# Kernel optimization log

Hardware: AMD Instinct MI355X
Metric: run time of the kernel (lower is better)

Reference implementation:

```python
import jax, jax.numpy as jnp
import numpy as np

DIM = 768
N_HEADS = 12
HEAD_DIM = DIM // N_HEADS
SCALE = HEAD_DIM ** -0.5


def setup_inputs() -> dict:
    key = jax.random.key(0)
    ks = jax.random.split(key, 5)
    x = jax.random.normal(ks[0], (8, 1024, DIM), dtype=jnp.float32)
    w_qkv = jax.random.normal(ks[1], (DIM, 3 * DIM), dtype=jnp.float32) * (DIM ** -0.5)
    b_qkv = jnp.zeros((3 * DIM,), dtype=jnp.float32)
    w_proj = jax.random.normal(ks[2], (DIM, DIM), dtype=jnp.float32) * (DIM ** -0.5)
    b_proj = jnp.zeros((DIM,), dtype=jnp.float32)
    return {"x": x, "w_qkv": w_qkv, "b_qkv": b_qkv, "w_proj": w_proj, "b_proj": b_proj}


def reference(x, w_qkv, b_qkv, w_proj, b_proj):
    B, N, _ = x.shape
    qkv = x @ w_qkv + b_qkv                       # [B, N, 3*DIM]
    qkv = qkv.reshape(B, N, 3, N_HEADS, HEAD_DIM)
    q = qkv[:, :, 0].transpose(0, 2, 1, 3)        # [B, H, N, D]
    k = qkv[:, :, 1].transpose(0, 2, 1, 3)
    v = qkv[:, :, 2].transpose(0, 2, 1, 3)
    attn = jnp.einsum('bhnd,bhmd->bhnm', q, k) * SCALE
    attn = jax.nn.softmax(attn, axis=-1)
    out = jnp.einsum('bhnm,bhmd->bhnd', attn, v)  # [B, H, N, D]
    out = out.transpose(0, 2, 1, 3).reshape(B, N, DIM)
    return out @ w_proj + b_proj
```

## Files before the change

kernel.cpp:

```cpp
#include <hip/hip_runtime.h>
#include <hip/hip_bf16.h>

#define NHEADS 12
#define HDIM   64
#define SEQ    1024
#define NBATCH 8
#define MODELD 768
#define QKVD   2304
#define BHEADS (NBATCH * NHEADS)

typedef __attribute__((ext_vector_type(8))) short          bf16x8;
typedef __attribute__((ext_vector_type(8))) unsigned short u16x8;
typedef __attribute__((ext_vector_type(4))) unsigned short u16x4;
typedef __attribute__((ext_vector_type(4))) float          f32x4;

static __device__ __forceinline__ unsigned short f2bf(float f) {
  unsigned int u = __float_as_uint(f);
  u += 0x7fffu + ((u >> 16) & 1u);
  return (unsigned short)(u >> 16);
}

static __device__ __forceinline__ unsigned int pk2(float x, float y) {
  __hip_bfloat162 h = __float22bfloat162_rn(make_float2(x, y));
  return *(unsigned int*)&h;
}

static __device__ __forceinline__ void gld_lds16(const void* g, void* l) {
  __builtin_amdgcn_global_load_lds((const __attribute__((address_space(1))) void*)g,
                                   (__attribute__((address_space(3))) void*)l, 16, 0, 0);
}

#define QSC 0.18033688f

__global__ __launch_bounds__(256) void convert_x(
    const float* __restrict__ in, unsigned short* __restrict__ out) {
  const int i = (blockIdx.x * 256 + threadIdx.x) * 8;
  const float4 a0 = *(const float4*)(in + i);
  const float4 a1 = *(const float4*)(in + i + 4);
  union { unsigned int u[4]; u16x8 v; } w;
  w.u[0] = pk2(a0.x, a0.y); w.u[1] = pk2(a0.z, a0.w);
  w.u[2] = pk2(a1.x, a1.y); w.u[3] = pk2(a1.z, a1.w);
  *(u16x8*)(out + i) = w.v;
}

__global__ __launch_bounds__(256) void transpose_f32_to_bf16(
    const float* __restrict__ in, unsigned short* __restrict__ out, int R, int C) {
  __shared__ float t[32][33];
  const int c0 = blockIdx.x * 32, r0 = blockIdx.y * 32;
  const int lr = threadIdx.x >> 3;
  const int lc = (threadIdx.x & 7) * 4;
  const float* p = in + (size_t)(r0 + lr) * C + c0 + lc;
  float4 v = *(const float4*)p;
  t[lr][lc]     = v.x;
  t[lr][lc + 1] = v.y;
  t[lr][lc + 2] = v.z;
  t[lr][lc + 3] = v.w;
  __syncthreads();
  unsigned short* q = out + (size_t)(c0 + lr) * R + r0 + lc;
  q[0] = f2bf(t[lc][lr]);
  q[1] = f2bf(t[lc + 1][lr]);
  q[2] = f2bf(t[lc + 2][lr]);
  q[3] = f2bf(t[lc + 3][lr]);
}

__global__ __launch_bounds__(512) void gemm_qkv(
    const unsigned short* __restrict__ Xb, const unsigned short* __restrict__ WT,
    const float* __restrict__ bias,
    unsigned short* __restrict__ Qo, unsigned short* __restrict__ Ko,
    unsigned short* __restrict__ VTo) {
  __shared__ __align__(16) unsigned short smem[49152];
  const int tid  = threadIdx.x;
  const int lane = tid & 63;
  const int wave = tid >> 6;
  int flat = blockIdx.x;
  flat = (flat & 7) * 72 + (flat >> 3);
  const int m0 = (flat / 18) * 256;
  const int n0 = (flat % 18) * 128;
  const int wrm = (wave >> 1) * 64;
  const int wcn = (wave & 1) * 64;
  const int srow = lane >> 3;
  const int scol = (((lane & 7) ^ srow) << 4);
  const int fr = lane & 15;
  const int fq = lane >> 4;
  const int swz = (fr & 7) << 4;

  const char* Ab = (const char*)(Xb + (size_t)m0 * MODELD);
  const char* Bb = (const char*)(WT + (size_t)n0 * MODELD);

  f32x4 acc[4][4] = {};

  auto stage = [&](int buf, int k0) {
#pragma unroll
    for (int u = 0; u < 4; ++u) {
      const int i = wave * 4 + u;
      const size_t roff = (size_t)(i * 8 + srow) * (MODELD * 2) + k0 * 2 + scol;
      gld_lds16(Ab + roff, (char*)smem + buf * 32768 + i * 1024);
    }
#pragma unroll
    for (int u = 0; u < 2; ++u) {
      const int i = wave * 2 + u;
      const size_t roff = (size_t)(i * 8 + srow) * (MODELD * 2) + k0 * 2 + scol;
      gld_lds16(Bb + roff, (char*)smem + 65536 + buf * 16384 + i * 1024);
    }
  };

  stage(0, 0);

  for (int t = 0; t < 12; ++t) {
    const int cur = t & 1;
    if (t < 11) {
      stage(cur ^ 1, (t + 1) * 64);
      asm volatile("s_waitcnt vmcnt(6)" ::: "memory");
    } else {
      asm volatile("s_waitcnt vmcnt(0)" ::: "memory");
    }
    __builtin_amdgcn_s_barrier();

    const char* Ac = (const char*)smem + cur * 32768;
    const char* Bc = (const char*)smem + 65536 + cur * 16384;
#pragma unroll
    for (int c = 0; c < 2; ++c) {
      const int cb = (c * 64 + fq * 16);
      bf16x8 af[4], bfr[4];
#pragma unroll
      for (int i = 0; i < 4; ++i) {
        af[i]  = *(const bf16x8*)(Ac + (wrm + i * 16 + fr) * 128 + (cb ^ swz));
        bfr[i] = *(const bf16x8*)(Bc + (wcn + i * 16 + fr) * 128 + (cb ^ swz));
      }
      __builtin_amdgcn_s_setprio(1);
#pragma unroll
      for (int i = 0; i < 4; ++i)
#pragma unroll
        for (int j = 0; j < 4; ++j)
          acc[i][j] = __builtin_amdgcn_mfma_f32_16x16x32_bf16(af[i], bfr[j], acc[i][j], 0, 0, 0);
      __builtin_amdgcn_s_setprio(0);
    }
    __builtin_amdgcn_s_barrier();
  }

  const int s = n0 / MODELD;
  if (s < 2) {
    const float qs = (s == 0) ? QSC : 1.0f;
#pragma unroll
    for (int i = 0; i < 4; ++i) {
#pragma unroll
      for (int j = 0; j < 4; ++j) {
        const int col = n0 + wcn + j * 16 + fr;
        const int rem = col - s * MODELD;
        const int h = rem >> 6, d = rem & 63;
        const float bv = bias[col];
#pragma unroll
        for (int r = 0; r < 4; ++r) {
          const int row = m0 + wrm + i * 16 + fq * 4 + r;
          const int b = row >> 10, n = row & 1023;
          const int bh = b * NHEADS + h;
          const unsigned short val = f2bf((acc[i][j][r] + bv) * qs);
          if (s == 0) Qo[((size_t)bh * SEQ + n) * HDIM + d] = val;
          else        Ko[((size_t)bh * SEQ + n) * HDIM + d] = val;
        }
      }
    }
  } else {
    unsigned short* T = smem + wave * 4608;
#pragma unroll
    for (int i = 0; i < 4; ++i) {
#pragma unroll
      for (int j = 0; j < 4; ++j) {
        const int col = n0 + wcn + j * 16 + fr;
        const float bv = bias[col];
        const int dl = j * 16 + fr;
        union { unsigned int u[2]; u16x4 v; } pk;
        pk.u[0] = pk2(acc[i][j][0] + bv, acc[i][j][1] + bv);
        pk.u[1] = pk2(acc[i][j][2] + bv, acc[i][j][3] + bv);
        *(u16x4*)&T[dl * 72 + i * 16 + fq * 4] = pk.v;
      }
    }
    asm volatile("s_waitcnt lgkmcnt(0)" ::: "memory");
    const int h  = (n0 + wcn - 2 * MODELD) >> 6;
    const int rowb = m0 + wrm;
    const int b  = rowb >> 10, nq = rowb & 1023;
    const int bh = b * NHEADS + h;
    unsigned short* Vb = VTo + ((size_t)bh * HDIM) * SEQ + nq;
#pragma unroll
    for (int u = 0; u < 8; ++u) {
      const int d  = u * 8 + (lane >> 3);
      const int qc = (lane & 7) * 8;
      u16x8 v = *(const u16x8*)&T[d * 72 + qc];
      *(u16x8*)(Vb + (size_t)d * SEQ + qc) = v;
    }
  }
}

__global__ __launch_bounds__(256, 3) void attn_fused(
    const unsigned short* __restrict__ Q, const unsigned short* __restrict__ K,
    const unsigned short* __restrict__ VT, unsigned short* __restrict__ AO) {
  __shared__ unsigned short Ks[2][64][64];
  __shared__ unsigned short Vs[2][64][64];

  const int tid  = threadIdx.x;
  const int lane = tid & 63;
  const int wave = tid >> 6;

  const int flat = blockIdx.y * 8 + blockIdx.x;
  const int xcd = flat & 7, j = flat >> 3;
  const int bh = xcd * 12 + (j >> 3);
  const int qb = j & 7;
  const int b = bh / NHEADS, h = bh % NHEADS;
  const int q0 = qb * 128 + wave * 32;

  const unsigned short* Qp = Q  + (size_t)bh * SEQ * HDIM;
  const unsigned short* Kp = K  + (size_t)bh * SEQ * HDIM;
  const unsigned short* Vp = VT + (size_t)bh * HDIM * SEQ;

  const int fr = lane & 15;
  const int fq = lane >> 4;
  const int swz = (fr & 7) << 4;

  bf16x8 qf[2][2];
#pragma unroll
  for (int g = 0; g < 2; ++g)
#pragma unroll
    for (int c = 0; c < 2; ++c)
      qf[g][c] = *(const bf16x8*)(Qp + (size_t)(q0 + g * 16 + fr) * HDIM + c * 32 + fq * 8);

  const int srow_lo = (lane >> 3);
  const int scx = (((lane & 7) ^ srow_lo) << 4);

  f32x4 acc[2][4] = {};
  f32x4 accl[2] = {};
  bf16x8 ones;
#pragma unroll
  for (int i = 0; i < 8; ++i) ones[i] = (short)0x3F80;

  auto stage = [&](int buf, int kv0) {
    const char* Kb = (const char*)Kp + (size_t)kv0 * 128;
    const char* Vb = (const char*)Vp + (size_t)kv0 * 2;
    char* dK = (char*)&Ks[buf][0][0];
    char* dV = (char*)&Vs[buf][0][0];
#pragma unroll
    for (int u = 0; u < 2; ++u) {
      const int i = wave * 2 + u;
      const int r0 = i * 8 + srow_lo;
      gld_lds16(Kb + (size_t)r0 * 128  + scx, dK + i * 1024);
      gld_lds16(Vb + (size_t)r0 * 2048 + scx, dV + i * 1024);
    }
  };

  stage(0, 0);

  for (int t = 0; t < SEQ / 64; ++t) {
    const int cur = t & 1;
    if (t < SEQ / 64 - 1) {
      stage(cur ^ 1, (t + 1) * 64);
      asm volatile("s_waitcnt vmcnt(4)" ::: "memory");
    } else {
      asm volatile("s_waitcnt vmcnt(0)" ::: "memory");
    }
    __builtin_amdgcn_s_barrier();

    const char* Kt = (const char*)&Ks[cur][0][0];
    const char* Vt = (const char*)&Vs[cur][0][0];

    bf16x8 kf[4][2];
#pragma unroll
    for (int ng = 0; ng < 4; ++ng)
#pragma unroll
      for (int c = 0; c < 2; ++c)
        kf[ng][c] = *(const bf16x8*)(Kt + (ng * 16 + fr) * 128 + ((c * 64 + fq * 16) ^ swz));

    f32x4 S[2][4] = {};
    __builtin_amdgcn_s_setprio(1);
#pragma unroll
    for (int g = 0; g < 2; ++g)
#pragma unroll
      for (int ng = 0; ng < 4; ++ng)
#pragma unroll
        for (int c = 0; c < 2; ++c)
          S[g][ng] = __builtin_amdgcn_mfma_f32_16x16x32_bf16(kf[ng][c], qf[g][c], S[g][ng], 0, 0, 0);
    __builtin_amdgcn_s_setprio(0);

    bf16x8 pf[2][2];
#pragma unroll
    for (int g = 0; g < 2; ++g) {
      unsigned int u[4][2];
#pragma unroll
      for (int ng = 0; ng < 4; ++ng) {
        const float p0 = __builtin_amdgcn_exp2f(S[g][ng][0]);
        const float p1 = __builtin_amdgcn_exp2f(S[g][ng][1]);
        const float p2 = __builtin_amdgcn_exp2f(S[g][ng][2]);
        const float p3 = __builtin_amdgcn_exp2f(S[g][ng][3]);
        u[ng][0] = pk2(p0, p1);
        u[ng][1] = pk2(p2, p3);
      }
#pragma unroll
      for (int c = 0; c < 2; ++c) {
        union { unsigned int w[4]; bf16x8 v; } pp;
#pragma unroll
        for (int d2 = 0; d2 < 2; ++d2) {
          unsigned int e = u[2 * c][d2], o = u[2 * c + 1][d2];
          asm("v_permlane32_swap_b32 %0, %1" : "+v"(e), "+v"(o));
          asm("v_permlane16_swap_b32 %0, %1" : "+v"(e), "+v"(o));
          pp.w[d2] = e;
          pp.w[2 + d2] = o;
        }
        pf[g][c] = pp.v;
      }
    }

    bf16x8 vf[4][2];
#pragma unroll
    for (int df = 0; df < 4; ++df)
#pragma unroll
      for (int c = 0; c < 2; ++c)
        vf[df][c] = *(const bf16x8*)(Vt + (df * 16 + fr) * 128 + ((c * 64 + fq * 16) ^ swz));

    __builtin_amdgcn_s_setprio(1);
#pragma unroll
    for (int g = 0; g < 2; ++g) {
#pragma unroll
      for (int df = 0; df < 4; ++df)
#pragma unroll
        for (int c = 0; c < 2; ++c)
          acc[g][df] = __builtin_amdgcn_mfma_f32_16x16x32_bf16(pf[g][c], vf[df][c], acc[g][df], 0, 0, 0);
#pragma unroll
      for (int c = 0; c < 2; ++c)
        accl[g] = __builtin_amdgcn_mfma_f32_16x16x32_bf16(pf[g][c], ones, accl[g], 0, 0, 0);
    }
    __builtin_amdgcn_s_setprio(0);

    __builtin_amdgcn_s_barrier();
  }

#pragma unroll
  for (int g = 0; g < 2; ++g) {
#pragma unroll
    for (int r = 0; r < 4; ++r) {
      const float inv = 1.0f / accl[g][r];
      const int q = q0 + g * 16 + fq * 4 + r;
      unsigned short* outp = AO + ((size_t)b * SEQ + q) * MODELD + h * HDIM;
#pragma unroll
      for (int df = 0; df < 4; ++df)
        outp[df * 16 + fr] = f2bf(acc[g][df][r] * inv);
    }
  }
}

__global__ __launch_bounds__(512) void gemm_proj(
    const unsigned short* __restrict__ A, const unsigned short* __restrict__ WT,
    const float* __restrict__ bias, float* __restrict__ Out) {
  __shared__ __align__(16) unsigned short smem[49152];
  const int tid  = threadIdx.x;
  const int lane = tid & 63;
  const int wave = tid >> 6;
  int flat = blockIdx.x;
  flat = (flat & 7) * 24 + (flat >> 3);
  const int m0 = (flat / 6) * 256;
  const int n0 = (flat % 6) * 128;
  const int wrm = (wave >> 1) * 64;
  const int wcn = (wave & 1) * 64;
  const int srow = lane >> 3;
  const int scol = (((lane & 7) ^ srow) << 4);
  const int fr = lane & 15;
  const int fq = lane >> 4;
  const int swz = (fr & 7) << 4;

  const char* Ab = (const char*)(A  + (size_t)m0 * MODELD);
  const char* Bb = (const char*)(WT + (size_t)n0 * MODELD);

  f32x4 acc[4][4] = {};

  auto stage = [&](int buf, int k0) {
#pragma unroll
    for (int u = 0; u < 4; ++u) {
      const int i = wave * 4 + u;
      const size_t roff = (size_t)(i * 8 + srow) * (MODELD * 2) + k0 * 2 + scol;
      gld_lds16(Ab + roff, (char*)smem + buf * 32768 + i * 1024);
    }
#pragma unroll
    for (int u = 0; u < 2; ++u) {
      const int i = wave * 2 + u;
      const size_t roff = (size_t)(i * 8 + srow) * (MODELD * 2) + k0 * 2 + scol;
      gld_lds16(Bb + roff, (char*)smem + 65536 + buf * 16384 + i * 1024);
    }
  };

  stage(0, 0);

  for (int t = 0; t < 12; ++t) {
    const int cur = t & 1;
    if (t < 11) {
      stage(cur ^ 1, (t + 1) * 64);
      asm volatile("s_waitcnt vmcnt(6)" ::: "memory");
    } else {
      asm volatile("s_waitcnt vmcnt(0)" ::: "memory");
    }
    __builtin_amdgcn_s_barrier();

    const char* Ac = (const char*)smem + cur * 32768;
    const char* Bc = (const char*)smem + 65536 + cur * 16384;
#pragma unroll
    for (int c = 0; c < 2; ++c) {
      const int cb = (c * 64 + fq * 16);
      bf16x8 af[4], bfr[4];
#pragma unroll
      for (int i = 0; i < 4; ++i) {
        af[i]  = *(const bf16x8*)(Ac + (wrm + i * 16 + fr) * 128 + (cb ^ swz));
        bfr[i] = *(const bf16x8*)(Bc + (wcn + i * 16 + fr) * 128 + (cb ^ swz));
      }
      __builtin_amdgcn_s_setprio(1);
#pragma unroll
      for (int i = 0; i < 4; ++i)
#pragma unroll
        for (int j = 0; j < 4; ++j)
          acc[i][j] = __builtin_amdgcn_mfma_f32_16x16x32_bf16(af[i], bfr[j], acc[i][j], 0, 0, 0);
      __builtin_amdgcn_s_setprio(0);
    }
    __builtin_amdgcn_s_barrier();
  }

#pragma unroll
  for (int i = 0; i < 4; ++i) {
#pragma unroll
    for (int j = 0; j < 4; ++j) {
      const int col = n0 + wcn + j * 16 + fr;
      const float bv = bias[col];
#pragma unroll
      for (int r = 0; r < 4; ++r) {
        const int row = m0 + wrm + i * 16 + fq * 4 + r;
        Out[(size_t)row * MODELD + col] = acc[i][j][r] + bv;
      }
    }
  }
}

extern "C" void kernel_launch(void* const* d_in, const int* in_sizes, int n_in,
                              void* d_out, int out_size, void* d_ws, size_t ws_size,
                              hipStream_t stream) {
  const float* x      = (const float*)d_in[0];
  const float* w_qkv  = (const float*)d_in[1];
  const float* b_qkv  = (const float*)d_in[2];
  const float* w_proj = (const float*)d_in[3];
  const float* b_proj = (const float*)d_in[4];
  float* out = (float*)d_out;

  unsigned short* ws = (unsigned short*)d_ws;
  unsigned short* wqkvT  = ws;
  unsigned short* wprojT = wqkvT + (size_t)QKVD * MODELD;
  unsigned short* Qw     = wprojT + (size_t)MODELD * MODELD;
  unsigned short* Kw     = Qw + (size_t)BHEADS * SEQ * HDIM;
  unsigned short* VTw    = Kw + (size_t)BHEADS * SEQ * HDIM;
  unsigned short* AO     = VTw + (size_t)BHEADS * SEQ * HDIM;
  unsigned short* Xb     = AO + (size_t)NBATCH * SEQ * MODELD;

  convert_x<<<dim3((NBATCH * SEQ * MODELD) / (256 * 8)), 256, 0, stream>>>(x, Xb);
  transpose_f32_to_bf16<<<dim3(QKVD / 32, MODELD / 32), 256, 0, stream>>>(
      w_qkv, wqkvT, MODELD, QKVD);
  transpose_f32_to_bf16<<<dim3(MODELD / 32, MODELD / 32), 256, 0, stream>>>(
      w_proj, wprojT, MODELD, MODELD);
  gemm_qkv<<<dim3((QKVD / 128) * ((NBATCH * SEQ) / 256)), 512, 0, stream>>>(
      Xb, wqkvT, b_qkv, Qw, Kw, VTw);
  attn_fused<<<dim3(SEQ / 128, BHEADS), 256, 0, stream>>>(Qw, Kw, VTw, AO);
  gemm_proj<<<dim3((MODELD / 128) * ((NBATCH * SEQ) / 256)), 512, 0, stream>>>(
      AO, wprojT, b_proj, out);
}
```

Before: 110.4 us.

## Triple-buffer LDS pipelines in GEMMs and attention; merge prep kernels into one launch

The QKV GEMM, the projection GEMM and the attention kernel move from double-buffered to triple-buffered LDS staging. Each iteration now prefetches two tiles ahead and drops one of its two barriers, since the buffer being refilled was read one iteration earlier. The three preprocessing kernels (convert x to bf16, transpose the two weight matrices) are folded into a single launch that dispatches on block index, saving two kernel launches. The cost is more LDS per block: the GEMMs go to about 144KB, which still fits one 512-thread block per CU, and attention goes to 48KB per block.

```diff
diff --git a/kernel.cpp b/kernel.cpp
--- a/kernel.cpp
+++ b/kernel.cpp
@@ -32,23 +32,13 @@
 
 #define QSC 0.18033688f
 
-__global__ __launch_bounds__(256) void convert_x(
-    const float* __restrict__ in, unsigned short* __restrict__ out) {
-  const int i = (blockIdx.x * 256 + threadIdx.x) * 8;
-  const float4 a0 = *(const float4*)(in + i);
-  const float4 a1 = *(const float4*)(in + i + 4);
-  union { unsigned int u[4]; u16x8 v; } w;
-  w.u[0] = pk2(a0.x, a0.y); w.u[1] = pk2(a0.z, a0.w);
-  w.u[2] = pk2(a1.x, a1.y); w.u[3] = pk2(a1.z, a1.w);
-  *(u16x8*)(out + i) = w.v;
-}
-
-__global__ __launch_bounds__(256) void transpose_f32_to_bf16(
-    const float* __restrict__ in, unsigned short* __restrict__ out, int R, int C) {
+static __device__ __forceinline__ void transpose_body(
+    const float* __restrict__ in, unsigned short* __restrict__ out,
+    int R, int C, int bx, int by, int tid) {
   __shared__ float t[32][33];
-  const int c0 = blockIdx.x * 32, r0 = blockIdx.y * 32;
-  const int lr = threadIdx.x >> 3;
-  const int lc = (threadIdx.x & 7) * 4;
+  const int c0 = bx * 32, r0 = by * 32;
+  const int lr = tid >> 3;
+  const int lc = (tid & 7) * 4;
   const float* p = in + (size_t)(r0 + lr) * C + c0 + lc;
   float4 v = *(const float4*)p;
   t[lr][lc]     = v.x;
@@ -63,12 +53,35 @@
   q[3] = f2bf(t[lc + 3][lr]);
 }
 
+__global__ __launch_bounds__(256) void prep(
+    const float* __restrict__ x, unsigned short* __restrict__ Xb,
+    const float* __restrict__ w_qkv, unsigned short* __restrict__ wqkvT,
+    const float* __restrict__ w_proj, unsigned short* __restrict__ wprojT) {
+  const int id = blockIdx.x;
+  const int tid = threadIdx.x;
+  if (id < 3072) {
+    const int i = (id * 256 + tid) * 8;
+    const float4 a0 = *(const float4*)(x + i);
+    const float4 a1 = *(const float4*)(x + i + 4);
+    union { unsigned int u[4]; u16x8 v; } w;
+    w.u[0] = pk2(a0.x, a0.y); w.u[1] = pk2(a0.z, a0.w);
+    w.u[2] = pk2(a1.x, a1.y); w.u[3] = pk2(a1.z, a1.w);
+    *(u16x8*)(Xb + i) = w.v;
+  } else if (id < 4800) {
+    const int u = id - 3072;
+    transpose_body(w_qkv, wqkvT, MODELD, QKVD, u % 72, u / 72, tid);
+  } else {
+    const int u = id - 4800;
+    transpose_body(w_proj, wprojT, MODELD, MODELD, u % 24, u / 24, tid);
+  }
+}
+
 __global__ __launch_bounds__(512) void gemm_qkv(
     const unsigned short* __restrict__ Xb, const unsigned short* __restrict__ WT,
     const float* __restrict__ bias,
     unsigned short* __restrict__ Qo, unsigned short* __restrict__ Ko,
     unsigned short* __restrict__ VTo) {
-  __shared__ __align__(16) unsigned short smem[49152];
+  __shared__ __align__(16) unsigned short smem[73728];
   const int tid  = threadIdx.x;
   const int lane = tid & 63;
   const int wave = tid >> 6;
@@ -100,24 +113,25 @@
     for (int u = 0; u < 2; ++u) {
       const int i = wave * 2 + u;
       const size_t roff = (size_t)(i * 8 + srow) * (MODELD * 2) + k0 * 2 + scol;
-      gld_lds16(Bb + roff, (char*)smem + 65536 + buf * 16384 + i * 1024);
+      gld_lds16(Bb + roff, (char*)smem + 98304 + buf * 16384 + i * 1024);
     }
   };
 
   stage(0, 0);
-
+  stage(1, 64);
+
+  int cur = 0;
   for (int t = 0; t < 12; ++t) {
-    const int cur = t & 1;
-    if (t < 11) {
-      stage(cur ^ 1, (t + 1) * 64);
-      asm volatile("s_waitcnt vmcnt(6)" ::: "memory");
-    } else {
-      asm volatile("s_waitcnt vmcnt(0)" ::: "memory");
-    }
+    if (t < 11) asm volatile("s_waitcnt vmcnt(6)" ::: "memory");
+    else        asm volatile("s_waitcnt vmcnt(0)" ::: "memory");
     __builtin_amdgcn_s_barrier();
+    if (t < 10) {
+      int sb = cur + 2; if (sb >= 3) sb -= 3;
+      stage(sb, (t + 2) * 64);
+    }
 
     const char* Ac = (const char*)smem + cur * 32768;
-    const char* Bc = (const char*)smem + 65536 + cur * 16384;
+    const char* Bc = (const char*)smem + 98304 + cur * 16384;
 #pragma unroll
     for (int c = 0; c < 2; ++c) {
       const int cb = (c * 64 + fq * 16);
@@ -135,8 +149,9 @@
           acc[i][j] = __builtin_amdgcn_mfma_f32_16x16x32_bf16(af[i], bfr[j], acc[i][j], 0, 0, 0);
       __builtin_amdgcn_s_setprio(0);
     }
-    __builtin_amdgcn_s_barrier();
-  }
+    cur = (cur == 2) ? 0 : cur + 1;
+  }
+  __builtin_amdgcn_s_barrier();
 
   const int s = n0 / MODELD;
   if (s < 2) {
@@ -194,8 +209,7 @@
 __global__ __launch_bounds__(256, 3) void attn_fused(
     const unsigned short* __restrict__ Q, const unsigned short* __restrict__ K,
     const unsigned short* __restrict__ VT, unsigned short* __restrict__ AO) {
-  __shared__ unsigned short Ks[2][64][64];
-  __shared__ unsigned short Vs[2][64][64];
+  __shared__ __align__(16) unsigned short smem[24576];
 
   const int tid  = threadIdx.x;
   const int lane = tid & 63;
@@ -235,31 +249,30 @@
   auto stage = [&](int buf, int kv0) {
     const char* Kb = (const char*)Kp + (size_t)kv0 * 128;
     const char* Vb = (const char*)Vp + (size_t)kv0 * 2;
-    char* dK = (char*)&Ks[buf][0][0];
-    char* dV = (char*)&Vs[buf][0][0];
 #pragma unroll
     for (int u = 0; u < 2; ++u) {
       const int i = wave * 2 + u;
       const int r0 = i * 8 + srow_lo;
-      gld_lds16(Kb + (size_t)r0 * 128  + scx, dK + i * 1024);
-      gld_lds16(Vb + (size_t)r0 * 2048 + scx, dV + i * 1024);
+      gld_lds16(Kb + (size_t)r0 * 128  + scx, (char*)smem + buf * 8192 + i * 1024);
+      gld_lds16(Vb + (size_t)r0 * 2048 + scx, (char*)smem + 24576 + buf * 8192 + i * 1024);
     }
   };
 
   stage(0, 0);
-
+  stage(1, 64);
+
+  int cur = 0;
   for (int t = 0; t < SEQ / 64; ++t) {
-    const int cur = t & 1;
-    if (t < SEQ / 64 - 1) {
-      stage(cur ^ 1, (t + 1) * 64);
-      asm volatile("s_waitcnt vmcnt(4)" ::: "memory");
-    } else {
-      asm volatile("s_waitcnt vmcnt(0)" ::: "memory");
-    }
+    if (t < SEQ / 64 - 1) asm volatile("s_waitcnt vmcnt(4)" ::: "memory");
+    else                  asm volatile("s_waitcnt vmcnt(0)" ::: "memory");
     __builtin_amdgcn_s_barrier();
-
-    const char* Kt = (const char*)&Ks[cur][0][0];
-    const char* Vt = (const char*)&Vs[cur][0][0];
+    if (t < SEQ / 64 - 2) {
+      int sb = cur + 2; if (sb >= 3) sb -= 3;
+      stage(sb, (t + 2) * 64);
+    }
+
+    const char* Kt = (const char*)smem + cur * 8192;
+    const char* Vt = (const char*)smem + 24576 + cur * 8192;
 
     bf16x8 kf[4][2];
 #pragma unroll
@@ -328,7 +341,7 @@
     }
     __builtin_amdgcn_s_setprio(0);
 
-    __builtin_amdgcn_s_barrier();
+    cur = (cur == 2) ? 0 : cur + 1;
   }
 
 #pragma unroll
@@ -348,7 +361,7 @@
 __global__ __launch_bounds__(512) void gemm_proj(
     const unsigned short* __restrict__ A, const unsigned short* __restrict__ WT,
     const float* __restrict__ bias, float* __restrict__ Out) {
-  __shared__ __align__(16) unsigned short smem[49152];
+  __shared__ __align__(16) unsigned short smem[73728];
   const int tid  = threadIdx.x;
   const int lane = tid & 63;
   const int wave = tid >> 6;
@@ -380,24 +393,25 @@
     for (int u = 0; u < 2; ++u) {
       const int i = wave * 2 + u;
       const size_t roff = (size_t)(i * 8 + srow) * (MODELD * 2) + k0 * 2 + scol;
-      gld_lds16(Bb + roff, (char*)smem + 65536 + buf * 16384 + i * 1024);
+      gld_lds16(Bb + roff, (char*)smem + 98304 + buf * 16384 + i * 1024);
     }
   };
 
   stage(0, 0);
-
+  stage(1, 64);
+
+  int cur = 0;
   for (int t = 0; t < 12; ++t) {
-    const int cur = t & 1;
-    if (t < 11) {
-      stage(cur ^ 1, (t + 1) * 64);
-      asm volatile("s_waitcnt vmcnt(6)" ::: "memory");
-    } else {
-      asm volatile("s_waitcnt vmcnt(0)" ::: "memory");
-    }
+    if (t < 11) asm volatile("s_waitcnt vmcnt(6)" ::: "memory");
+    else        asm volatile("s_waitcnt vmcnt(0)" ::: "memory");
     __builtin_amdgcn_s_barrier();
+    if (t < 10) {
+      int sb = cur + 2; if (sb >= 3) sb -= 3;
+      stage(sb, (t + 2) * 64);
+    }
 
     const char* Ac = (const char*)smem + cur * 32768;
-    const char* Bc = (const char*)smem + 65536 + cur * 16384;
+    const char* Bc = (const char*)smem + 98304 + cur * 16384;
 #pragma unroll
     for (int c = 0; c < 2; ++c) {
       const int cb = (c * 64 + fq * 16);
@@ -415,7 +429,7 @@
           acc[i][j] = __builtin_amdgcn_mfma_f32_16x16x32_bf16(af[i], bfr[j], acc[i][j], 0, 0, 0);
       __builtin_amdgcn_s_setprio(0);
     }
-    __builtin_amdgcn_s_barrier();
+    cur = (cur == 2) ? 0 : cur + 1;
   }
 
 #pragma unroll
@@ -452,11 +466,7 @@
   unsigned short* AO     = VTw + (size_t)BHEADS * SEQ * HDIM;
   unsigned short* Xb     = AO + (size_t)NBATCH * SEQ * MODELD;
 
-  convert_x<<<dim3((NBATCH * SEQ * MODELD) / (256 * 8)), 256, 0, stream>>>(x, Xb);
-  transpose_f32_to_bf16<<<dim3(QKVD / 32, MODELD / 32), 256, 0, stream>>>(
-      w_qkv, wqkvT, MODELD, QKVD);
-  transpose_f32_to_bf16<<<dim3(MODELD / 32, MODELD / 32), 256, 0, stream>>>(
-      w_proj, wprojT, MODELD, MODELD);
+  prep<<<dim3(5376), 256, 0, stream>>>(x, Xb, w_qkv, wqkvT, w_proj, wprojT);
   gemm_qkv<<<dim3((QKVD / 128) * ((NBATCH * SEQ) / 256)), 512, 0, stream>>>(
       Xb, wqkvT, b_qkv, Qw, Kw, VTw);
   attn_fused<<<dim3(SEQ / 128, BHEADS), 256, 0, stream>>>(Qw, Kw, VTw, AO);
```

Measured after the change: 103.2 us. -6.6%, faster.
